# Performance work log

Hardware: AMD Instinct MI355X
Metric: run time of the kernel (lower is better)

Reference implementation:

```python
import jax, jax.numpy as jnp
import numpy as np

B, S, F = 16, 511, 128           # batch, input seq len, n_features
D, H, NB = 512, 8, 6             # embedding_dim, n_heads, n_blocks
DH = D // H                      # d_head
MLP = 4 * D                      # mlp_ratio=4 hard-coded in FxtBlock
OUT = 1                          # out_d
T = S + 1                        # tokens incl. cls
EPS = 1e-5                       # torch LayerNorm default eps


def pos_emb(seq_len, d):
    # matches get_positional_embeddings: sin for even j, cos for odd j (with j-1 exponent)
    i = np.arange(seq_len, dtype=np.float32)[:, None]
    j = np.arange(d)
    je = np.where(j % 2 == 0, j, j - 1).astype(np.float32)
    ang = i / (10000.0 ** (je / d))
    pe = np.where(j % 2 == 0, np.sin(ang), np.cos(ang))
    return jnp.asarray(pe, jnp.float32)


def layernorm(x, g, b):
    m = jnp.mean(x, axis=-1, keepdims=True)
    v = jnp.mean((x - m) ** 2, axis=-1, keepdims=True)
    return (x - m) * jax.lax.rsqrt(v + EPS) * g + b


def setup_inputs() -> dict:
    key = jax.random.key(0)
    ks = jax.random.split(key, 12)
    g = lambda k, shape: jax.random.normal(k, shape, jnp.float32) * 0.02
    return {
        "src": jax.random.normal(ks[0], (B, S, F), jnp.float32),
        "emb_W": g(ks[1], (F, D)), "emb_b": jnp.zeros((D,), jnp.float32),
        "cls_tok": jax.random.uniform(ks[2], (1, D), jnp.float32),
        "ln1_g": jnp.ones((NB, D), jnp.float32), "ln1_b": jnp.zeros((NB, D), jnp.float32),
        "Wq": g(ks[3], (NB, H, DH, DH)), "bq": jnp.zeros((NB, H, DH), jnp.float32),
        "Wk": g(ks[4], (NB, H, DH, DH)), "bk": jnp.zeros((NB, H, DH), jnp.float32),
        "Wv": g(ks[5], (NB, H, DH, DH)), "bv": jnp.zeros((NB, H, DH), jnp.float32),
        "ln2_g": jnp.ones((NB, D), jnp.float32), "ln2_b": jnp.zeros((NB, D), jnp.float32),
        "W1": g(ks[6], (NB, D, MLP)), "b1": jnp.zeros((NB, MLP), jnp.float32),
        "W2": g(ks[7], (NB, MLP, D)), "b2": jnp.zeros((NB, D), jnp.float32),
        "head_W": g(ks[8], (D, OUT)), "head_b": jnp.zeros((OUT,), jnp.float32),
    }


def reference(src, emb_W, emb_b, cls_tok, ln1_g, ln1_b, Wq, bq, Wk, bk, Wv, bv,
              ln2_g, ln2_b, W1, b1, W2, b2, head_W, head_b):
    b = src.shape[0]
    x = src @ emb_W + emb_b                                    # [B,S,D]
    cls = jnp.broadcast_to(cls_tok[None], (b, 1, D))
    x = jnp.concatenate([cls, x], axis=1) + pos_emb(T, D)[None]  # [B,T,D]
    scale = 1.0 / jnp.sqrt(jnp.float32(DH))
    for i in range(NB):
        h = layernorm(x, ln1_g[i], ln1_b[i])
        hh = h.reshape(b, T, H, DH)
        q = jnp.einsum('bthd,hde->bhte', hh, Wq[i]) + bq[i][None, :, None, :]
        k = jnp.einsum('bthd,hde->bhte', hh, Wk[i]) + bk[i][None, :, None, :]
        v = jnp.einsum('bthd,hde->bhte', hh, Wv[i]) + bv[i][None, :, None, :]
        attn = jax.nn.softmax(jnp.einsum('bhse,bhte->bhst', q, k) * scale, axis=-1)
        o = jnp.einsum('bhst,bhte->bhse', attn, v)             # [B,H,T,DH]
        x = x + o.transpose(0, 2, 1, 3).reshape(b, T, D)
        h2 = layernorm(x, ln2_g[i], ln2_b[i])
        x = x + (jax.nn.gelu(h2 @ W1[i] + b1[i], approximate=False) @ W2[i] + b2[i])
    return jax.nn.sigmoid(x[:, 0] @ head_W + head_b)           # [B,OUT]
```

## Files before the change

### kernel.cpp

```cpp
#include <hip/hip_runtime.h>
#include <hip/hip_bf16.h>
#include <math.h>

#define B 16
#define S 511
#define F 128
#define D 512
#define H 8
#define NB 6
#define DH 64
#define MLPD 2048
#define T 512
#define EPS 1e-5f

typedef unsigned short ushort;
typedef __attribute__((ext_vector_type(8))) short short8;
typedef __attribute__((ext_vector_type(4))) float floatx4;

__device__ __forceinline__ ushort f2bf(float f) {
    union { float f; unsigned u; } cv; cv.f = f;
    unsigned r = (cv.u + 0x7fff + ((cv.u >> 16) & 1)) >> 16;
    return (ushort)r;
}

__device__ __forceinline__ float fast_gelu(float x) {
    float z = fabsf(x) * 0.70710678118f;
    float t = 1.0f / (1.0f + 0.3275911f * z);
    float p = ((((1.061405429f * t - 1.453152027f) * t + 1.421413741f) * t
               - 0.284496736f) * t + 0.254829592f) * t;
    float erfv = 1.0f - p * __expf(-z * z);
    erfv = copysignf(erfv, x);
    return 0.5f * x * (1.0f + erfv);
}

__global__ void castsrc_kernel(const float* __restrict__ src, ushort* __restrict__ srcb) {
    int row = blockIdx.x;
    int t = row & (T - 1), b = row >> 9;
    int tid = threadIdx.x;
    ushort v = 0;
    if (t > 0) v = f2bf(src[((size_t)b * S + (t - 1)) * F + tid]);
    srcb[(size_t)row * F + tid] = v;
}

__global__ void wtrans_kernel(const float* __restrict__ W,
                              ushort* __restrict__ Wt,
                              int K, int N) {
    int kb = blockIdx.x * 32, nb = blockIdx.y * 32, mat = blockIdx.z;
    __shared__ float tile[32][33];
    int tid = threadIdx.x;
    int c = tid & 31, r0 = tid >> 5;
    const float* Wm = W + (size_t)mat * K * N;
    ushort* Wtm = Wt + (size_t)mat * K * N;
    #pragma unroll
    for (int l = 0; l < 4; ++l) {
        int r = r0 + l * 8;
        tile[r][c] = Wm[(size_t)(kb + r) * N + nb + c];
    }
    __syncthreads();
    #pragma unroll
    for (int l = 0; l < 4; ++l) {
        int r = r0 + l * 8;
        Wtm[(size_t)(nb + r) * K + kb + c] = f2bf(tile[c][r]);
    }
}

__global__ void wtransq_kernel(const float* __restrict__ Wq, const float* __restrict__ Wk,
                               const float* __restrict__ Wv,
                               ushort* __restrict__ WqT, ushort* __restrict__ WkT,
                               ushort* __restrict__ WvT) {
    int mat = blockIdx.x;
    int which = blockIdx.y;
    const float* W = (which == 0 ? Wq : which == 1 ? Wk : Wv) + (size_t)mat * 4096;
    ushort* O = (which == 0 ? WqT : which == 1 ? WkT : WvT) + (size_t)mat * 4096;
    __shared__ float t[64][65];
    int tid = threadIdx.x;
    int r0 = tid >> 6, c = tid & 63;
    #pragma unroll
    for (int l = 0; l < 16; ++l) {
        int row = r0 * 16 + l;
        t[row][c] = W[row * 64 + c];
    }
    __syncthreads();
    #pragma unroll
    for (int l = 0; l < 16; ++l) {
        int row = r0 * 16 + l;
        O[row * 64 + c] = f2bf(t[c][row]);
    }
}

__device__ __forceinline__ void gload_lds16(const ushort* g, ushort* l) {
    __builtin_amdgcn_global_load_lds((const __attribute__((address_space(1))) unsigned int*)g,
                                     (__attribute__((address_space(3))) unsigned int*)l,
                                     16, 0, 0);
}

#define S_WAITCNT_VM(N) asm volatile("s_waitcnt vmcnt(" #N ")" ::: "memory")

__global__ __launch_bounds__(256) void embed_gemm(const ushort* __restrict__ A,
                                                  const ushort* __restrict__ Bt,
                                                  const float* __restrict__ emb_b,
                                                  const float* __restrict__ cls_tok,
                                                  float* __restrict__ x) {
    __shared__ ushort As[64 * 32];
    __shared__ ushort Bs[64 * 32];
    int tid = threadIdx.x;
    int lane = tid & 63;
    int w = __builtin_amdgcn_readfirstlane(tid >> 6);
    int quad = lane >> 4, l15 = lane & 15;
    int wr = (w >> 1) * 32, wc = (w & 1) * 32;
    int m0 = blockIdx.x * 64, n0 = blockIdx.y * 64;

    floatx4 acc[2][2];
    #pragma unroll
    for (int i = 0; i < 2; ++i)
        #pragma unroll
        for (int j = 0; j < 2; ++j) acc[i][j] = (floatx4)0.f;

    int lrow = lane >> 2;
    int lk = (lane & 3) * 8;
    const ushort* Ag = A + (size_t)(m0 + 16 * w + lrow) * F + lk;
    const ushort* Bg = Bt + (size_t)(n0 + 16 * w + lrow) * F + lk;
    ushort* AsW = &As[16 * w * 32];
    ushort* BsW = &Bs[16 * w * 32];
    int fa = l15 * 32 + quad * 8;

    for (int kt = 0; kt < F; kt += 32) {
        gload_lds16(Ag + kt, AsW);
        gload_lds16(Bg + kt, BsW);
        __syncthreads();
        short8 af[2], bf[2];
        #pragma unroll
        for (int i = 0; i < 2; ++i) af[i] = *(const short8*)&As[(wr + 16 * i) * 32 + fa];
        #pragma unroll
        for (int j = 0; j < 2; ++j) bf[j] = *(const short8*)&Bs[(wc + 16 * j) * 32 + fa];
        #pragma unroll
        for (int i = 0; i < 2; ++i)
            #pragma unroll
            for (int j = 0; j < 2; ++j)
                acc[i][j] = __builtin_amdgcn_mfma_f32_16x16x32_bf16(af[i], bf[j], acc[i][j], 0, 0, 0);
        __syncthreads();
    }

    const float LOG1E4 = 9.210340371976184f;
    int rbase = (lane >> 4) * 4;
    int cidx = lane & 15;
    #pragma unroll
    for (int j = 0; j < 2; ++j) {
        int gc = n0 + wc + 16 * j + cidx;
        float je = (float)(gc & ~1);
        float freq = expf(-(je / (float)D) * LOG1E4);
        float ebv = emb_b[gc];
        float clsv = cls_tok[gc];
        bool odd = (gc & 1);
        #pragma unroll
        for (int i = 0; i < 2; ++i) {
            int gr = m0 + wr + 16 * i + rbase;
            #pragma unroll
            for (int reg = 0; reg < 4; ++reg) {
                int row = gr + reg;
                int t = row & (T - 1);
                float ang = (float)t * freq;
                float pe = odd ? cosf(ang) : sinf(ang);
                float val = (t == 0) ? (clsv + pe) : (acc[i][j][reg] + ebv + pe);
                x[(size_t)row * D + gc] = val;
            }
        }
    }
}

__global__ __launch_bounds__(256) void ln_kernel(const float* __restrict__ xin,
                                                 const float* __restrict__ g,
                                                 const float* __restrict__ bb,
                                                 ushort* __restrict__ out) {
    int lane = threadIdx.x & 63;
    int row = blockIdx.x * 4 + (threadIdx.x >> 6);
    const float* xr = xin + (size_t)row * D + lane * 8;
    float4 a0 = *(const float4*)xr;
    float4 a1 = *(const float4*)(xr + 4);
    float s = a0.x + a0.y + a0.z + a0.w + a1.x + a1.y + a1.z + a1.w;
    #pragma unroll
    for (int off = 1; off < 64; off <<= 1) s += __shfl_xor(s, off);
    float mean = s * (1.0f / (float)D);
    float d0 = a0.x - mean, d1 = a0.y - mean, d2 = a0.z - mean, d3 = a0.w - mean;
    float d4 = a1.x - mean, d5 = a1.y - mean, d6 = a1.z - mean, d7 = a1.w - mean;
    float sq = d0*d0 + d1*d1 + d2*d2 + d3*d3 + d4*d4 + d5*d5 + d6*d6 + d7*d7;
    #pragma unroll
    for (int off = 1; off < 64; off <<= 1) sq += __shfl_xor(sq, off);
    float rstd = rsqrtf(sq * (1.0f / (float)D) + EPS);
    const float* gp = g + lane * 8;
    const float* bp = bb + lane * 8;
    float4 g0 = *(const float4*)gp, g1 = *(const float4*)(gp + 4);
    float4 b0 = *(const float4*)bp, b1 = *(const float4*)(bp + 4);
    short8 o;
    o[0] = (short)f2bf(d0 * rstd * g0.x + b0.x);
    o[1] = (short)f2bf(d1 * rstd * g0.y + b0.y);
    o[2] = (short)f2bf(d2 * rstd * g0.z + b0.z);
    o[3] = (short)f2bf(d3 * rstd * g0.w + b0.w);
    o[4] = (short)f2bf(d4 * rstd * g1.x + b1.x);
    o[5] = (short)f2bf(d5 * rstd * g1.y + b1.y);
    o[6] = (short)f2bf(d6 * rstd * g1.z + b1.z);
    o[7] = (short)f2bf(d7 * rstd * g1.w + b1.w);
    *(short8*)(out + (size_t)row * D + lane * 8) = o;
}

#define LQPAD 520
__global__ __launch_bounds__(256) void lnqkv_kernel(
        const float* __restrict__ x,
        const float* __restrict__ g, const float* __restrict__ bb,
        const ushort* __restrict__ WqT, const float* __restrict__ bq,
        const ushort* __restrict__ WkT, const float* __restrict__ bk,
        const ushort* __restrict__ WvT, const float* __restrict__ bv,
        ushort* __restrict__ qo, ushort* __restrict__ ko, ushort* __restrict__ vTo) {
    __shared__ ushort hl[32 * LQPAD];
    int tid = threadIdx.x;
    int lane = tid & 63;
    int w = __builtin_amdgcn_readfirstlane(tid >> 6);
    int quad = lane >> 4, l15 = lane & 15;
    int m0 = blockIdx.x * 32;

    for (int it = 0; it < 8; ++it) {
        int lr = it * 4 + w;
        const float* xr = x + (size_t)(m0 + lr) * D + lane * 8;
        float4 a0 = *(const float4*)xr;
        float4 a1 = *(const float4*)(xr + 4);
        float s = a0.x + a0.y + a0.z + a0.w + a1.x + a1.y + a1.z + a1.w;
        #pragma unroll
        for (int off = 1; off < 64; off <<= 1) s += __shfl_xor(s, off);
        float mean = s * (1.0f / (float)D);
        float d0 = a0.x - mean, d1 = a0.y - mean, d2 = a0.z - mean, d3 = a0.w - mean;
        float d4 = a1.x - mean, d5 = a1.y - mean, d6 = a1.z - mean, d7 = a1.w - mean;
        float sq = d0*d0 + d1*d1 + d2*d2 + d3*d3 + d4*d4 + d5*d5 + d6*d6 + d7*d7;
        #pragma unroll
        for (int off = 1; off < 64; off <<= 1) sq += __shfl_xor(sq, off);
        float rstd = rsqrtf(sq * (1.0f / (float)D) + EPS);
        const float* gp = g + lane * 8;
        const float* bp = bb + lane * 8;
        float4 g0 = *(const float4*)gp, g1 = *(const float4*)(gp + 4);
        float4 b0 = *(const float4*)bp, b1v = *(const float4*)(bp + 4);
        short8 o;
        o[0] = (short)f2bf(d0 * rstd * g0.x + b0.x);
        o[1] = (short)f2bf(d1 * rstd * g0.y + b0.y);
        o[2] = (short)f2bf(d2 * rstd * g0.z + b0.z);
        o[3] = (short)f2bf(d3 * rstd * g0.w + b0.w);
        o[4] = (short)f2bf(d4 * rstd * g1.x + b1v.x);
        o[5] = (short)f2bf(d5 * rstd * g1.y + b1v.y);
        o[6] = (short)f2bf(d6 * rstd * g1.z + b1v.z);
        o[7] = (short)f2bf(d7 * rstd * g1.w + b1v.w);
        *(short8*)(hl + lr * LQPAD + lane * 8) = o;
    }
    __syncthreads();

    int bb_ = m0 >> 9;
    #pragma unroll
    for (int hp = 0; hp < 2; ++hp) {
        int hh = w * 2 + hp;
        short8 af[2][2];
        #pragma unroll
        for (int mt = 0; mt < 2; ++mt)
            #pragma unroll
            for (int ks = 0; ks < 2; ++ks)
                af[mt][ks] = *(const short8*)&hl[(mt * 16 + l15) * LQPAD + hh * DH + ks * 32 + quad * 8];

        floatx4 acc[3][2][4];
        #pragma unroll
        for (int xo = 0; xo < 3; ++xo)
            #pragma unroll
            for (int mt = 0; mt < 2; ++mt)
                #pragma unroll
                for (int nt = 0; nt < 4; ++nt) acc[xo][mt][nt] = (floatx4)0.f;

        #pragma unroll
        for (int xo = 0; xo < 3; ++xo) {
            const ushort* WT = (xo == 0 ? WqT : xo == 1 ? WkT : WvT) + (size_t)hh * 4096;
            #pragma unroll
            for (int nt = 0; nt < 4; ++nt) {
                const ushort* wb = WT + (size_t)(nt * 16 + l15) * 64 + quad * 8;
                short8 bf0 = *(const short8*)(wb);
                short8 bf1 = *(const short8*)(wb + 32);
                #pragma unroll
                for (int mt = 0; mt < 2; ++mt) {
                    acc[xo][mt][nt] = __builtin_amdgcn_mfma_f32_16x16x32_bf16(af[mt][0], bf0, acc[xo][mt][nt], 0, 0, 0);
                    acc[xo][mt][nt] = __builtin_amdgcn_mfma_f32_16x16x32_bf16(af[mt][1], bf1, acc[xo][mt][nt], 0, 0, 0);
                }
            }
        }

        int bh = bb_ * H + hh;
        #pragma unroll
        for (int mt = 0; mt < 2; ++mt) {
            int trow = m0 + mt * 16 + quad * 4;
            int tt = trow & (T - 1);
            #pragma unroll
            for (int nt = 0; nt < 4; ++nt) {
                int col = nt * 16 + l15;
                float bqv = bq[hh * DH + col];
                float bkv = bk[hh * DH + col];
                float bvv = bv[hh * DH + col];
                #pragma unroll
                for (int reg = 0; reg < 4; ++reg) {
                    qo[((size_t)bh * T + tt + reg) * DH + col] = f2bf(acc[0][mt][nt][reg] + bqv);
                    ko[((size_t)bh * T + tt + reg) * DH + col] = f2bf(acc[1][mt][nt][reg] + bkv);
                    vTo[((size_t)bh * DH + col) * T + tt + reg] = f2bf(acc[2][mt][nt][reg] + bvv);
                }
            }
        }
    }
}

#define PSTRIDE 88
__global__ __launch_bounds__(256) void attn_kernel(const ushort* __restrict__ q,
                                                   const ushort* __restrict__ k,
                                                   const ushort* __restrict__ vT,
                                                   float* __restrict__ x) {
    int bh = blockIdx.x;
    int qt = blockIdx.y;
    int b = bh >> 3, hh = bh & 7;
    int tid = threadIdx.x;
    int lane = tid & 63;
    int w = __builtin_amdgcn_readfirstlane(tid >> 6);
    int quad = lane >> 4, l15 = lane & 15;

    __shared__ __align__(16) ushort smem[22016];
    ushort* Pw = smem + 16384 + w * (16 * PSTRIDE);

    const ushort* qbase = q + ((size_t)bh * T + qt * 64 + w * 16 + l15) * DH + quad * 8;
    short8 Qf0 = *(const short8*)(qbase);
    short8 Qf1 = *(const short8*)(qbase + 32);

    const ushort* kbase = k + (size_t)bh * T * DH;
    const ushort* vbase = vT + (size_t)bh * DH * T;

    int srow = lane >> 2;
    int scol = (lane & 3) * 8;
    const ushort* kg = kbase + (size_t)(w * 16 + srow) * DH + scol;
    const ushort* vg = vbase + (size_t)(w * 16 + srow) * T + scol;
    ushort* ldsK = smem + w * 16 * 32;
    ushort* ldsV = smem + 8192 + w * 16 * 32;

    float l_i[4] = {0.f, 0.f, 0.f, 0.f};
    floatx4 O[4];
    #pragma unroll
    for (int j = 0; j < 4; ++j) O[j] = (floatx4)0.f;

    gload_lds16(kg, ldsK);
    gload_lds16(kg + 32, ldsK + 2048);
    gload_lds16(vg, ldsV);
    gload_lds16(vg + 32, ldsV + 2048);
    __syncthreads();

    for (int kt = 0; kt < T / 64; ++kt) {
        int cur = kt & 1;
        if (kt < T / 64 - 1) {
            int nb = cur ^ 1;
            const ushort* kgn = kg + (size_t)(kt + 1) * 64 * DH;
            const ushort* vgn = vg + (kt + 1) * 64;
            gload_lds16(kgn, ldsK + nb * 4096);
            gload_lds16(kgn + 32, ldsK + nb * 4096 + 2048);
            gload_lds16(vgn, ldsV + nb * 4096);
            gload_lds16(vgn + 32, ldsV + nb * 4096 + 2048);
        }
        const ushort* Kc = smem + cur * 4096;
        const ushort* Vc = smem + 8192 + cur * 4096;

        floatx4 sc[4];
        __builtin_amdgcn_s_setprio(1);
        #pragma unroll
        for (int j = 0; j < 4; ++j) {
            int ro = (j * 16 + l15) * 32 + quad * 8;
            short8 kf0 = *(const short8*)&Kc[ro];
            short8 kf1 = *(const short8*)&Kc[2048 + ro];
            floatx4 s4 = (floatx4)0.f;
            s4 = __builtin_amdgcn_mfma_f32_16x16x32_bf16(Qf0, kf0, s4, 0, 0, 0);
            s4 = __builtin_amdgcn_mfma_f32_16x16x32_bf16(Qf1, kf1, s4, 0, 0, 0);
            sc[j] = s4;
        }
        __builtin_amdgcn_s_setprio(0);
        #pragma unroll
        for (int j = 0; j < 4; ++j) {
            #pragma unroll
            for (int r = 0; r < 4; ++r) {
                float p = __expf(sc[j][r] * 0.125f);
                l_i[r] += p;
                Pw[(quad * 4 + r) * PSTRIDE + j * 16 + l15] = f2bf(p);
            }
        }

        short8 af0 = *(const short8*)&Pw[l15 * PSTRIDE + quad * 8];
        short8 af1 = *(const short8*)&Pw[l15 * PSTRIDE + 32 + quad * 8];
        __builtin_amdgcn_s_setprio(1);
        #pragma unroll
        for (int j = 0; j < 4; ++j) {
            int ro = (j * 16 + l15) * 32 + quad * 8;
            short8 vf0 = *(const short8*)&Vc[ro];
            short8 vf1 = *(const short8*)&Vc[2048 + ro];
            O[j] = __builtin_amdgcn_mfma_f32_16x16x32_bf16(af0, vf0, O[j], 0, 0, 0);
            O[j] = __builtin_amdgcn_mfma_f32_16x16x32_bf16(af1, vf1, O[j], 0, 0, 0);
        }
        __builtin_amdgcn_s_setprio(0);
        __syncthreads();
    }

    #pragma unroll
    for (int r = 0; r < 4; ++r) {
        l_i[r] += __shfl_xor(l_i[r], 1);
        l_i[r] += __shfl_xor(l_i[r], 2);
        l_i[r] += __shfl_xor(l_i[r], 4);
        l_i[r] += __shfl_xor(l_i[r], 8);
    }

    float* Ow = (float*)smem + w * 16 * 68;
    #pragma unroll
    for (int r = 0; r < 4; ++r) {
        float rl = 1.0f / l_i[r];
        #pragma unroll
        for (int j = 0; j < 4; ++j)
            Ow[(quad * 4 + r) * 68 + j * 16 + l15] = O[j][r] * rl;
    }
    __syncthreads();
    int r4 = lane >> 4;
    int c16 = lane & 15;
    #pragma unroll
    for (int i = 0; i < 4; ++i) {
        int lrow = i * 4 + r4;
        float4 o = *(const float4*)&Ow[lrow * 68 + c16 * 4];
        int grow = qt * 64 + w * 16 + lrow;
        float* xp = &x[((size_t)(b * T) + grow) * D + hh * DH + c16 * 4];
        float4 xv = *(const float4*)xp;
        xv.x += o.x; xv.y += o.y; xv.z += o.z; xv.w += o.w;
        *(float4*)xp = xv;
    }
}

template<int BM, int EPI>
__global__ __launch_bounds__(512) void gemm_pipe(const ushort* __restrict__ A,
                                                 const ushort* __restrict__ Bt,
                                                 const float* __restrict__ bias,
                                                 void* __restrict__ Cout,
                                                 int N, int K) {
    constexpr int BN = 128;
    constexpr int BK = 64;
    constexpr int MREP = BM / 32;
    constexpr int AJ = BM / 64;
    constexpr int TILE = (BM + BN) * BK;
    __shared__ ushort lds[3 * TILE];

    int tid = threadIdx.x;
    int lane = tid & 63;
    int w = __builtin_amdgcn_readfirstlane(tid >> 6);
    int quad = lane >> 4, l15 = lane & 15;
    int wrow = (w >> 2) * (BM / 2);
    int wcol = (w & 3) * 32;
    int m0 = blockIdx.x * BM, n0 = blockIdx.y * BN;

    int lrow8 = lane >> 3;
    int lslot = lane & 7;
    int scol = (lslot ^ lrow8) * 8;
    const ushort* Asrc = A + (size_t)(m0 + w * 8 + lrow8) * K + scol;
    const ushort* Bsrc = Bt + (size_t)(n0 + w * 8 + lrow8) * K + scol;
    ushort* ldsA0 = lds + (w * 8) * BK;
    ushort* ldsB0 = lds + BM * BK + (w * 8) * BK;

    int sx0 = ((quad) ^ (l15 & 7)) * 8;
    int sx1 = ((4 + quad) ^ (l15 & 7)) * 8;

    floatx4 acc[MREP][2];
    #pragma unroll
    for (int i = 0; i < MREP; ++i) {
        acc[i][0] = (floatx4)0.f;
        acc[i][1] = (floatx4)0.f;
    }

    #define STAGE_T(t, buf) do {                                                   \
        const ushort* ap_ = Asrc + (size_t)(t) * BK;                               \
        const ushort* bp_ = Bsrc + (size_t)(t) * BK;                               \
        ushort* la_ = ldsA0 + (buf) * TILE;                                        \
        ushort* lb_ = ldsB0 + (buf) * TILE;                                        \
        _Pragma("unroll")                                                          \
        for (int j = 0; j < AJ; ++j)                                               \
            gload_lds16(ap_ + (size_t)j * 64 * K, la_ + j * 64 * BK);              \
        _Pragma("unroll")                                                          \
        for (int j = 0; j < 2; ++j)                                                \
            gload_lds16(bp_ + (size_t)j * 64 * K, lb_ + j * 64 * BK);              \
    } while (0)

    #define COMPUTE_T(buf) do {                                                    \
        const ushort* Ab_ = lds + (buf) * TILE;                                    \
        const ushort* Bb_ = Ab_ + BM * BK;                                         \
        _Pragma("unroll")                                                          \
        for (int ks = 0; ks < 2; ++ks) {                                           \
            int sx_ = ks ? sx1 : sx0;                                              \
            short8 bfr0 = *(const short8*)&Bb_[(wcol + l15) * BK + sx_];           \
            short8 bfr1 = *(const short8*)&Bb_[(wcol + 16 + l15) * BK + sx_];      \
            _Pragma("unroll")                                                      \
            for (int i = 0; i < MREP; ++i) {                                       \
                short8 af_ = *(const short8*)&Ab_[(wrow + i * 16 + l15) * BK + sx_]; \
                acc[i][0] = __builtin_amdgcn_mfma_f32_16x16x32_bf16(af_, bfr0, acc[i][0], 0, 0, 0); \
                acc[i][1] = __builtin_amdgcn_mfma_f32_16x16x32_bf16(af_, bfr1, acc[i][1], 0, 0, 0); \
            }                                                                      \
        }                                                                          \
    } while (0)

    STAGE_T(0, 0);
    STAGE_T(1, 1);

    int NT = K / BK;
    int cb = 0, nbuf = 2;
    for (int t = 0; t < NT - 2; ++t) {
        STAGE_T(t + 2, nbuf);
        if constexpr (AJ == 4) { S_WAITCNT_VM(12); } else { S_WAITCNT_VM(8); }
        __builtin_amdgcn_s_barrier();
        __builtin_amdgcn_s_setprio(1);
        COMPUTE_T(cb);
        __builtin_amdgcn_s_setprio(0);
        asm volatile("s_waitcnt lgkmcnt(0)" ::: "memory");
        __builtin_amdgcn_s_barrier();
        cb = (cb == 2) ? 0 : cb + 1;
        nbuf = (nbuf == 2) ? 0 : nbuf + 1;
    }
    if constexpr (AJ == 4) { S_WAITCNT_VM(6); } else { S_WAITCNT_VM(4); }
    __builtin_amdgcn_s_barrier();
    __builtin_amdgcn_s_setprio(1);
    COMPUTE_T(cb);
    __builtin_amdgcn_s_setprio(0);
    asm volatile("s_waitcnt lgkmcnt(0)" ::: "memory");
    __builtin_amdgcn_s_barrier();
    cb = (cb == 2) ? 0 : cb + 1;
    S_WAITCNT_VM(0);
    __builtin_amdgcn_s_barrier();
    COMPUTE_T(cb);

    #undef STAGE_T
    #undef COMPUTE_T

    int rbase = quad * 4;
    #pragma unroll
    for (int i = 0; i < MREP; ++i) {
        #pragma unroll
        for (int n = 0; n < 2; ++n) {
            int gc = n0 + wcol + n * 16 + l15;
            float bv = bias[gc];
            int gr = m0 + wrow + i * 16 + rbase;
            #pragma unroll
            for (int reg = 0; reg < 4; ++reg) {
                if constexpr (EPI == 0) {
                    ((ushort*)Cout)[(size_t)(gr + reg) * N + gc] =
                        f2bf(fast_gelu(acc[i][n][reg] + bv));
                } else if constexpr (EPI == 1) {
                    ((float*)Cout)[(size_t)(gr + reg) * N + gc] = acc[i][n][reg] + bv;
                } else {
                    float* xp = (float*)Cout + (size_t)(gr + reg) * N + gc;
                    *xp = *xp + acc[i][n][reg] + bv;
                }
            }
        }
    }
}

__global__ __launch_bounds__(256) void ln_cls_kernel(const float* __restrict__ x,
                                                     const float* __restrict__ g,
                                                     const float* __restrict__ bb,
                                                     ushort* __restrict__ h2c) {
    int lane = threadIdx.x & 63;
    int r = blockIdx.x * 4 + (threadIdx.x >> 6);
    const float* xr = x + (size_t)r * T * D + lane * 8;
    float4 a0 = *(const float4*)xr;
    float4 a1 = *(const float4*)(xr + 4);
    float s = a0.x + a0.y + a0.z + a0.w + a1.x + a1.y + a1.z + a1.w;
    #pragma unroll
    for (int off = 1; off < 64; off <<= 1) s += __shfl_xor(s, off);
    float mean = s * (1.0f / (float)D);
    float d0 = a0.x - mean, d1 = a0.y - mean, d2 = a0.z - mean, d3 = a0.w - mean;
    float d4 = a1.x - mean, d5 = a1.y - mean, d6 = a1.z - mean, d7 = a1.w - mean;
    float sq = d0*d0 + d1*d1 + d2*d2 + d3*d3 + d4*d4 + d5*d5 + d6*d6 + d7*d7;
    #pragma unroll
    for (int off = 1; off < 64; off <<= 1) sq += __shfl_xor(sq, off);
    float rstd = rsqrtf(sq * (1.0f / (float)D) + EPS);
    const float* gp = g + lane * 8;
    const float* bp = bb + lane * 8;
    float4 g0 = *(const float4*)gp, g1 = *(const float4*)(gp + 4);
    float4 b0 = *(const float4*)bp, b1v = *(const float4*)(bp + 4);
    short8 o;
    o[0] = (short)f2bf(d0 * rstd * g0.x + b0.x);
    o[1] = (short)f2bf(d1 * rstd * g0.y + b0.y);
    o[2] = (short)f2bf(d2 * rstd * g0.z + b0.z);
    o[3] = (short)f2bf(d3 * rstd * g0.w + b0.w);
    o[4] = (short)f2bf(d4 * rstd * g1.x + b1v.x);
    o[5] = (short)f2bf(d5 * rstd * g1.y + b1v.y);
    o[6] = (short)f2bf(d6 * rstd * g1.z + b1v.z);
    o[7] = (short)f2bf(d7 * rstd * g1.w + b1v.w);
    *(short8*)(h2c + r * D + lane * 8) = o;
}

__global__ __launch_bounds__(256) void gemm1_cls(const ushort* __restrict__ h2c,
                                                 const ushort* __restrict__ W1t,
                                                 const float* __restrict__ b1,
                                                 ushort* __restrict__ uc) {
    int tid = threadIdx.x;
    int lane = tid & 63;
    int w = __builtin_amdgcn_readfirstlane(tid >> 6);
    int quad = lane >> 4, l15 = lane & 15;
    int nb = blockIdx.x * 64 + w * 16;

    short8 af[16];
    #pragma unroll
    for (int ks = 0; ks < 16; ++ks)
        af[ks] = *(const short8*)&h2c[l15 * D + ks * 32 + quad * 8];

    const ushort* wrow = W1t + (size_t)(nb + l15) * D + quad * 8;
    floatx4 acc = (floatx4)0.f;
    #pragma unroll
    for (int ks = 0; ks < 16; ++ks) {
        short8 bf = *(const short8*)(wrow + ks * 32);
        acc = __builtin_amdgcn_mfma_f32_16x16x32_bf16(af[ks], bf, acc, 0, 0, 0);
    }
    float bv = b1[nb + l15];
    #pragma unroll
    for (int reg = 0; reg < 4; ++reg)
        uc[(size_t)(quad * 4 + reg) * MLPD + nb + l15] = f2bf(fast_gelu(acc[reg] + bv));
}

__global__ __launch_bounds__(256) void gemm2_cls(const ushort* __restrict__ uc,
                                                 const ushort* __restrict__ W2t,
                                                 const float* __restrict__ b2,
                                                 float* __restrict__ p0c) {
    __shared__ float red[4 * 256];
    int tid = threadIdx.x;
    int lane = tid & 63;
    int w = __builtin_amdgcn_readfirstlane(tid >> 6);
    int quad = lane >> 4, l15 = lane & 15;
    int nb = blockIdx.x * 16;

    const ushort* wrow = W2t + (size_t)(nb + l15) * MLPD + quad * 8;
    floatx4 acc = (floatx4)0.f;
    #pragma unroll
    for (int k8 = 0; k8 < 16; ++k8) {
        int ks = w * 16 + k8;
        short8 a2 = *(const short8*)&uc[(size_t)l15 * MLPD + ks * 32 + quad * 8];
        short8 bf = *(const short8*)(wrow + (size_t)ks * 32);
        acc = __builtin_amdgcn_mfma_f32_16x16x32_bf16(a2, bf, acc, 0, 0, 0);
    }
    #pragma unroll
    for (int reg = 0; reg < 4; ++reg)
        red[w * 256 + (quad * 4 + reg) * 16 + l15] = acc[reg];
    __syncthreads();
    int row = tid >> 4, col = tid & 15;
    float s = red[row * 16 + col] + red[256 + row * 16 + col]
            + red[512 + row * 16 + col] + red[768 + row * 16 + col];
    p0c[(size_t)row * D + nb + col] = s + b2[nb + col];
}

__global__ void head_kernel(const float* __restrict__ x,
                            const float* __restrict__ p0c,
                            const float* __restrict__ hw,
                            const float* __restrict__ hb,
                            float* __restrict__ out) {
    int b = blockIdx.x;
    int tid = threadIdx.x;
    float s = (x[(size_t)b * T * D + tid] + p0c[(size_t)b * D + tid]) * hw[tid];
    #pragma unroll
    for (int off = 32; off > 0; off >>= 1) s += __shfl_down(s, off, 64);
    __shared__ float red[8];
    if ((tid & 63) == 0) red[tid >> 6] = s;
    __syncthreads();
    if (tid == 0) {
        float t = 0.f;
        #pragma unroll
        for (int i = 0; i < 8; ++i) t += red[i];
        out[b] = 1.0f / (1.0f + __expf(-(t + hb[0])));
    }
}

extern "C" void kernel_launch(void* const* d_in, const int* in_sizes, int n_in,
                              void* d_out, int out_size, void* d_ws, size_t ws_size,
                              hipStream_t stream) {
    const float* src     = (const float*)d_in[0];
    const float* emb_W   = (const float*)d_in[1];
    const float* emb_b   = (const float*)d_in[2];
    const float* cls_tok = (const float*)d_in[3];
    const float* ln1_g   = (const float*)d_in[4];
    const float* ln1_b   = (const float*)d_in[5];
    const float* Wq      = (const float*)d_in[6];
    const float* bq      = (const float*)d_in[7];
    const float* Wk      = (const float*)d_in[8];
    const float* bk      = (const float*)d_in[9];
    const float* Wv      = (const float*)d_in[10];
    const float* bv      = (const float*)d_in[11];
    const float* ln2_g   = (const float*)d_in[12];
    const float* ln2_b   = (const float*)d_in[13];
    const float* W1      = (const float*)d_in[14];
    const float* b1      = (const float*)d_in[15];
    const float* W2      = (const float*)d_in[16];
    const float* b2      = (const float*)d_in[17];
    const float* head_W  = (const float*)d_in[18];
    const float* head_b  = (const float*)d_in[19];

    const size_t NTOK = (size_t)B * T;
    char* wsb = (char*)d_ws;
    float*  x    = (float*)wsb;      wsb += NTOK * D * 4;
    ushort* hbuf = (ushort*)wsb;     wsb += NTOK * D * 2;
    ushort* q    = (ushort*)wsb;     wsb += NTOK * D * 2;
    ushort* k    = (ushort*)wsb;     wsb += NTOK * D * 2;
    ushort* vT   = (ushort*)wsb;     wsb += NTOK * D * 2;
    ushort* u    = (ushort*)wsb;     wsb += NTOK * MLPD * 2;
    ushort* W1t  = (ushort*)wsb;     wsb += (size_t)NB * D * MLPD * 2;
    ushort* W2t  = (ushort*)wsb;     wsb += (size_t)NB * D * MLPD * 2;
    ushort* WqT  = (ushort*)wsb;     wsb += (size_t)NB * H * DH * DH * 2;
    ushort* WkT  = (ushort*)wsb;     wsb += (size_t)NB * H * DH * DH * 2;
    ushort* WvT  = (ushort*)wsb;     wsb += (size_t)NB * H * DH * DH * 2;
    ushort* srcb = (ushort*)wsb;     wsb += NTOK * F * 2;
    ushort* embWt= (ushort*)wsb;     wsb += (size_t)F * D * 2;
    ushort* h2c  = (ushort*)wsb;     wsb += (size_t)16 * D * 2;
    ushort* ucls = (ushort*)wsb;     wsb += (size_t)16 * MLPD * 2;
    float*  p0c  = (float*)wsb;      wsb += (size_t)16 * D * 4;

    wtrans_kernel<<<dim3(D / 32, MLPD / 32, NB), 256, 0, stream>>>(W1, W1t, D, MLPD);
    wtrans_kernel<<<dim3(MLPD / 32, D / 32, NB), 256, 0, stream>>>(W2, W2t, MLPD, D);
    wtransq_kernel<<<dim3(NB * H, 3), 256, 0, stream>>>(Wq, Wk, Wv, WqT, WkT, WvT);
    wtrans_kernel<<<dim3(F / 32, D / 32, 1), 256, 0, stream>>>(emb_W, embWt, F, D);
    castsrc_kernel<<<B * T, F, 0, stream>>>(src, srcb);

    embed_gemm<<<dim3(B * T / 64, D / 64), 256, 0, stream>>>(srcb, embWt, emb_b, cls_tok, x);

    for (int i = 0; i < NB; ++i) {
        lnqkv_kernel<<<B * T / 32, 256, 0, stream>>>(x,
            ln1_g + i * D, ln1_b + i * D,
            WqT + (size_t)i * H * DH * DH, bq + (size_t)i * H * DH,
            WkT + (size_t)i * H * DH * DH, bk + (size_t)i * H * DH,
            WvT + (size_t)i * H * DH * DH, bv + (size_t)i * H * DH,
            q, k, vT);
        if (i < NB - 1) {
            attn_kernel<<<dim3(B * H, T / 64), 256, 0, stream>>>(q, k, vT, x);
            ln_kernel<<<B * T / 4, 256, 0, stream>>>(x, ln2_g + i * D, ln2_b + i * D, hbuf);
            gemm_pipe<256, 0><<<dim3(B * T / 256, MLPD / 128), 512, 0, stream>>>(
                hbuf, W1t + (size_t)i * D * MLPD, b1 + (size_t)i * MLPD, u, MLPD, D);
            gemm_pipe<128, 2><<<dim3(B * T / 128, D / 128), 512, 0, stream>>>(
                u, W2t + (size_t)i * MLPD * D, b2 + (size_t)i * D, x, D, MLPD);
        } else {
            attn_kernel<<<dim3(B * H, 1), 256, 0, stream>>>(q, k, vT, x);
            ln_cls_kernel<<<4, 256, 0, stream>>>(x,
                ln2_g + (size_t)i * D, ln2_b + (size_t)i * D, h2c);
            gemm1_cls<<<MLPD / 64, 256, 0, stream>>>(h2c,
                W1t + (size_t)i * D * MLPD, b1 + (size_t)i * MLPD, ucls);
            gemm2_cls<<<D / 16, 256, 0, stream>>>(ucls,
                W2t + (size_t)i * MLPD * D, b2 + (size_t)i * D, p0c);
            head_kernel<<<B, 512, 0, stream>>>(x, p0c, head_W, head_b, (float*)d_out);
        }
    }
}
```

Measured before the change: 762.3 us.

## Add 256x256 ping-pong pipelined GEMM kernel for the first MLP projection

Result: no change. 753.5 us (-1.2%).

```diff
diff --git a/kernel.cpp b/kernel.cpp
--- a/kernel.cpp
+++ b/kernel.cpp
@@ -95,6 +95,8 @@
 }
 
 #define S_WAITCNT_VM(N) asm volatile("s_waitcnt vmcnt(" #N ")" ::: "memory")
+#define S_WAITCNT_LGKM0 asm volatile("s_waitcnt lgkmcnt(0)" ::: "memory")
+#define S_WAITCNT_LGKM8 asm volatile("s_waitcnt lgkmcnt(8)" ::: "memory")
 
 __global__ __launch_bounds__(256) void embed_gemm(const ushort* __restrict__ A,
                                                   const ushort* __restrict__ Bt,
@@ -428,6 +430,156 @@
         float4 xv = *(const float4*)xp;
         xv.x += o.x; xv.y += o.y; xv.z += o.z; xv.w += o.w;
         *(float4*)xp = xv;
+    }
+}
+
+__global__ __launch_bounds__(512, 1) void gemm1_8p(const ushort* __restrict__ A,
+                                                   const ushort* __restrict__ Bt,
+                                                   const float* __restrict__ bias,
+                                                   ushort* __restrict__ C,
+                                                   int N, int K) {
+    constexpr int BUF = 32768;
+    constexpr int BOFS = 16384;
+    __shared__ ushort lds[2 * BUF];
+
+    int tid = threadIdx.x;
+    int lane = tid & 63;
+    int w = __builtin_amdgcn_readfirstlane(tid >> 6);
+    int quad = lane >> 4, l15 = lane & 15;
+    int wm = w >> 2, wn = w & 3;
+    int wmr = wm * 128, wnr = wn * 64;
+
+    int nwg = gridDim.x;
+    int id = blockIdx.x;
+    int idx = (id & 7) * (nwg >> 3) + (id >> 3);
+    int NTg = N >> 8;
+    int mt = idx / NTg, nt = idx - mt * NTg;
+    int m0 = mt * 256, n0 = nt * 256;
+
+    int strow = tid >> 3;
+    int ssw = ((tid & 7) ^ (strow & 7)) * 8;
+    const ushort* Ag = A + (size_t)(m0 + strow) * K + ssw;
+    const ushort* Bg = Bt + (size_t)(n0 + strow) * K + ssw;
+    int wdst = w << 9;
+
+    int sx0 = (quad ^ (l15 & 7)) * 8;
+    int sx1 = ((4 + quad) ^ (l15 & 7)) * 8;
+
+    floatx4 acc[8][4];
+    #pragma unroll
+    for (int i = 0; i < 8; ++i)
+        #pragma unroll
+        for (int n = 0; n < 4; ++n) acc[i][n] = (floatx4)0.f;
+
+    short8 a[4][2], b[4][2];
+
+    #define STG_AH(h, t, bp) do {                                                         \
+        gload_lds16(Ag + (size_t)((h) * 128) * K + (size_t)(t) * 64,                      \
+                    (bp) + ((h) * 128) * 64 + wdst);                                      \
+        gload_lds16(Ag + (size_t)((h) * 128 + 64) * K + (size_t)(t) * 64,                 \
+                    (bp) + ((h) * 128 + 64) * 64 + wdst);                                 \
+    } while (0)
+    #define STG_BH(h, t, bp) do {                                                         \
+        gload_lds16(Bg + (size_t)((h) * 128) * K + (size_t)(t) * 64,                      \
+                    (bp) + BOFS + ((h) * 128) * 64 + wdst);                                \
+        gload_lds16(Bg + (size_t)((h) * 128 + 64) * K + (size_t)(t) * 64,                 \
+                    (bp) + BOFS + ((h) * 128 + 64) * 64 + wdst);                           \
+    } while (0)
+
+    #define RD_A03(bp) do { _Pragma("unroll")                                             \
+        for (int ks = 0; ks < 2; ++ks) { int sx = ks ? sx1 : sx0;                         \
+            _Pragma("unroll")                                                             \
+            for (int i = 0; i < 4; ++i)                                                   \
+                a[i][ks] = *(const short8*)&(bp)[(wmr + i * 16 + l15) * 64 + sx]; } } while (0)
+    #define RD_A47(bp) do { _Pragma("unroll")                                             \
+        for (int ks = 0; ks < 2; ++ks) { int sx = ks ? sx1 : sx0;                         \
+            _Pragma("unroll")                                                             \
+            for (int i = 0; i < 4; ++i)                                                   \
+                a[i][ks] = *(const short8*)&(bp)[(wmr + (4 + i) * 16 + l15) * 64 + sx]; } } while (0)
+    #define RD_B01(bp) do { _Pragma("unroll")                                             \
+        for (int ks = 0; ks < 2; ++ks) { int sx = ks ? sx1 : sx0;                         \
+            _Pragma("unroll")                                                             \
+            for (int n = 0; n < 2; ++n)                                                   \
+                b[n][ks] = *(const short8*)&(bp)[BOFS + (wnr + n * 16 + l15) * 64 + sx]; } } while (0)
+    #define RD_B23(bp) do { _Pragma("unroll")                                             \
+        for (int ks = 0; ks < 2; ++ks) { int sx = ks ? sx1 : sx0;                         \
+            _Pragma("unroll")                                                             \
+            for (int n = 0; n < 2; ++n)                                                   \
+                b[2 + n][ks] = *(const short8*)&(bp)[BOFS + (wnr + (2 + n) * 16 + l15) * 64 + sx]; } } while (0)
+
+    #define MFQ(mb, nb2) do { _Pragma("unroll")                                           \
+        for (int ks = 0; ks < 2; ++ks)                                                    \
+            _Pragma("unroll")                                                             \
+            for (int i = 0; i < 4; ++i)                                                   \
+                _Pragma("unroll")                                                         \
+                for (int n = 0; n < 2; ++n)                                               \
+                    acc[(mb) + i][(nb2) + n] = __builtin_amdgcn_mfma_f32_16x16x32_bf16(   \
+                        a[i][ks], b[(nb2) + n][ks], acc[(mb) + i][(nb2) + n], 0, 0, 0); } while (0)
+
+    #define BAR __builtin_amdgcn_s_barrier()
+    #define PRIO_MFQ(mb, nb2) do { __builtin_amdgcn_s_setprio(1); MFQ(mb, nb2);           \
+                                   __builtin_amdgcn_s_setprio(0); } while (0)
+
+    ushort* buf0 = lds;
+    ushort* buf1 = lds + BUF;
+
+    STG_AH(0, 0, buf0); STG_AH(1, 0, buf0); STG_BH(0, 0, buf0); STG_BH(1, 0, buf0);
+    STG_BH(0, 1, buf1); STG_BH(1, 1, buf1); STG_AH(0, 1, buf1);
+    S_WAITCNT_VM(6);
+    BAR;
+
+    int NITER = K >> 7;
+    int NT = K >> 6;
+    for (int it = 0; it < NITER; ++it) {
+        int t2 = 2 * it + 2, t3 = 2 * it + 3;
+        bool s2 = (t2 < NT);
+        RD_A03(buf0); RD_B01(buf0);
+        STG_AH(1, 2 * it + 1, buf1);
+        S_WAITCNT_LGKM8;
+        BAR; S_WAITCNT_LGKM0; PRIO_MFQ(0, 0); BAR;
+        RD_B23(buf0);
+        BAR; S_WAITCNT_LGKM0; PRIO_MFQ(0, 2); BAR;
+        RD_A47(buf0);
+        if (s2) { STG_BH(0, t2, buf0); STG_BH(1, t2, buf0); }
+        BAR; S_WAITCNT_LGKM0; PRIO_MFQ(4, 2); BAR;
+        if (s2) { STG_AH(0, t2, buf0); S_WAITCNT_VM(6); } else { S_WAITCNT_VM(0); }
+        BAR; PRIO_MFQ(4, 0); BAR;
+        RD_A03(buf1); RD_B01(buf1);
+        if (s2) STG_AH(1, t2, buf0);
+        S_WAITCNT_LGKM8;
+        BAR; S_WAITCNT_LGKM0; PRIO_MFQ(0, 0); BAR;
+        RD_B23(buf1);
+        BAR; S_WAITCNT_LGKM0; PRIO_MFQ(0, 2); BAR;
+        RD_A47(buf1);
+        if (s2) { STG_BH(0, t3, buf1); STG_BH(1, t3, buf1); }
+        BAR; S_WAITCNT_LGKM0; PRIO_MFQ(4, 2); BAR;
+        if (s2) { STG_AH(0, t3, buf1); S_WAITCNT_VM(6); }
+        BAR; PRIO_MFQ(4, 0); BAR;
+    }
+
+    #undef STG_AH
+    #undef STG_BH
+    #undef RD_A03
+    #undef RD_A47
+    #undef RD_B01
+    #undef RD_B23
+    #undef MFQ
+    #undef BAR
+    #undef PRIO_MFQ
+
+    int rbase = quad * 4;
+    #pragma unroll
+    for (int i = 0; i < 8; ++i) {
+        #pragma unroll
+        for (int n = 0; n < 4; ++n) {
+            int gc = n0 + wnr + n * 16 + l15;
+            float bv = bias[gc];
+            int gr = m0 + wmr + i * 16 + rbase;
+            #pragma unroll
+            for (int reg = 0; reg < 4; ++reg) {
+                C[(size_t)(gr + reg) * N + gc] = f2bf(fast_gelu(acc[i][n][reg] + bv));
+            }
+        }
     }
 }
 
@@ -731,7 +883,7 @@
         if (i < NB - 1) {
             attn_kernel<<<dim3(B * H, T / 64), 256, 0, stream>>>(q, k, vT, x);
             ln_kernel<<<B * T / 4, 256, 0, stream>>>(x, ln2_g + i * D, ln2_b + i * D, hbuf);
-            gemm_pipe<256, 0><<<dim3(B * T / 256, MLPD / 128), 512, 0, stream>>>(
+            gemm1_8p<<<dim3((B * T / 256) * (MLPD / 256)), 512, 0, stream>>>(
                 hbuf, W1t + (size_t)i * D * MLPD, b1 + (size_t)i * MLPD, u, MLPD, D);
             gemm_pipe<128, 2><<<dim3(B * T / 128, D / 128), 512, 0, stream>>>(
                 u, W2t + (size_t)i * MLPD * D, b2 + (size_t)i * D, x, D, MLPD);
```
